# Kernel tuning notes

Hardware: AMD Instinct MI355X
Metric: run time of the kernel (lower is better)

The kernel has to match this reference:

```python
import jax, jax.numpy as jnp
import numpy as np

N = 50000      # nodes
E = 500000     # edges
D_IN = 64      # node_in_dim
K = 4          # edge_in_dim
H = 64         # node_hidden_dim
C = 40         # num_class
L = 2          # num_layers


def setup_inputs() -> dict:
    key = jax.random.key(0)
    ks = jax.random.split(key, 10)
    node_features = jax.random.normal(ks[0], (N, D_IN), jnp.float32)
    edge_features = jax.random.normal(ks[1], (L, E, K), jnp.float32)
    src = jax.random.randint(ks[2], (E,), 0, N)
    dst = jax.random.randint(ks[3], (E,), 0, N)
    W0 = jax.random.normal(ks[4], (K * D_IN, H), jnp.float32) * 0.05
    b0 = jnp.zeros((H,), jnp.float32)
    W1 = jax.random.normal(ks[5], (K * H, H), jnp.float32) * 0.05
    b1 = jnp.zeros((H,), jnp.float32)
    Wfc = jax.random.normal(ks[6], (H, C), jnp.float32) * 0.05
    bfc = jnp.zeros((C,), jnp.float32)
    return dict(node_features=node_features, edge_features=edge_features,
                src=src, dst=dst, W0=W0, b0=b0, W1=W1, b1=b1, Wfc=Wfc, bfc=bfc)


def reference(node_features, edge_features, src, dst, W0, b0, W1, b1, Wfc, bfc):
    h = node_features  # [N, d]
    ones = jnp.ones((E,), jnp.float32)
    cnt = jnp.maximum(jax.ops.segment_sum(ones, dst, num_segments=N), 1.0)  # in-degree
    for i, (W, b) in enumerate([(W0, b0), (W1, b1)]):
        e = edge_features[i]          # [E, K]
        hs = h[src]                   # [E, d] edge gather of src node features
        d = hs.shape[1]
        # message: relu(Linear(flatten(e[:,:,None] * h[:,None,:])))
        # flatten order is (K, d), so reshape W -> [K, d, H] and contract directly
        Wr = W.reshape(K, d, H)
        m = jax.nn.relu(jnp.einsum('ek,ed,kdh->eh', e, hs, Wr) + b)  # [E, H]
        s = jax.ops.segment_sum(m, dst, num_segments=N)              # scatter-sum
        h = jax.nn.relu(s / cnt[:, None])                            # mailbox mean + relu
    return h @ Wfc + bfc  # [N, C]
```

## Files before the change

### kernel.cpp

```cpp
#include <hip/hip_runtime.h>
#include <hip/hip_fp16.h>

#define N_NODES 50000
#define N_EDGES 500000
#define DIM 64
#define KDIM 4
#define HID 64
#define NCLS 40
#define NBLK ((N_NODES + 255) / 256)

__device__ inline unsigned pack2(float a, float b) {
    __half2 h = __floats2half2_rn(a, b);
    return *(unsigned*)&h;
}
__device__ inline float2 unpack2(unsigned u) {
    __half2 h = *(__half2*)&u;
    return __half22float2(h);
}

__global__ void hist_k(const int* __restrict__ dst, int* __restrict__ cnt) {
    int e = blockIdx.x * 256 + threadIdx.x;
    if (e < N_EDGES) atomicAdd(&cnt[dst[e]], 1);
}

__global__ __launch_bounds__(256) void blk_scan_k(const int* __restrict__ cnt,
                                                  int* __restrict__ esc,
                                                  int* __restrict__ bsum) {
    __shared__ int ls[256];
    int t = threadIdx.x;
    int n = blockIdx.x * 256 + t;
    int v = (n < N_NODES) ? cnt[n] : 0;
    ls[t] = v;
    __syncthreads();
#pragma unroll
    for (int off = 1; off < 256; off <<= 1) {
        int u = (t >= off) ? ls[t - off] : 0;
        __syncthreads();
        ls[t] += u;
        __syncthreads();
    }
    if (n < N_NODES) esc[n] = ls[t] - v;
    if (t == 255) bsum[blockIdx.x] = ls[255];
}

__global__ __launch_bounds__(256) void bsum_scan_k(const int* __restrict__ bsum,
                                                   int* __restrict__ boff,
                                                   int* __restrict__ start) {
    __shared__ int ls[256];
    int t = threadIdx.x;
    int v = (t < NBLK) ? bsum[t] : 0;
    ls[t] = v;
    __syncthreads();
#pragma unroll
    for (int off = 1; off < 256; off <<= 1) {
        int u = (t >= off) ? ls[t - off] : 0;
        __syncthreads();
        ls[t] += u;
        __syncthreads();
    }
    if (t < NBLK) boff[t] = ls[t] - v;
    if (t == 0) start[N_NODES] = N_EDGES;
}

__global__ void finalize_k(const int* __restrict__ esc, const int* __restrict__ boff,
                           int* __restrict__ start, int* __restrict__ cursor) {
    int n = blockIdx.x * 256 + threadIdx.x;
    if (n < N_NODES) {
        int s = esc[n] + boff[blockIdx.x];
        start[n] = s;
        cursor[n] = s;
    }
}

__global__ void scatter_k(const int* __restrict__ src, const int* __restrict__ dst,
                          const float* __restrict__ ef, int* __restrict__ cursor,
                          uint4* __restrict__ rec0, uint4* __restrict__ rec1) {
    int e = blockIdx.x * 256 + threadIdx.x;
    if (e < N_EDGES) {
        int d = dst[e];
        int pos = atomicAdd(&cursor[d], 1);
        int sn = src[e];
        float4 f0 = ((const float4*)ef)[e];
        float4 f1 = ((const float4*)ef)[N_EDGES + e];
        uint4 r0 = make_uint4((unsigned)sn, pack2(f0.x, f0.y), pack2(f0.z, f0.w), 0u);
        uint4 r1 = make_uint4((unsigned)sn, pack2(f1.x, f1.y), pack2(f1.z, f1.w), 0u);
        rec0[pos] = r0;
        rec1[pos] = r1;
    }
}

__global__ __launch_bounds__(256) void transform_k(const float* __restrict__ hin,
                                                   const float* __restrict__ W,
                                                   unsigned* __restrict__ y) {
    __shared__ float sW[KDIM * 64 * 64];
    __shared__ float sh[32 * 65];
    int t = threadIdx.x;

    const float4* W4 = (const float4*)W;
    float4* sW4 = (float4*)sW;
#pragma unroll
    for (int i = 0; i < 16; ++i) sW4[t + 256 * i] = W4[t + 256 * i];

    int n0 = blockIdx.x * 32;
#pragma unroll
    for (int i = 0; i < 2; ++i) {
        int idx = t + 256 * i;
        int nl = idx >> 4;
        int dg = idx & 15;
        int n = n0 + nl;
        float4 v = make_float4(0.f, 0.f, 0.f, 0.f);
        if (n < N_NODES) v = ((const float4*)hin)[(size_t)n * 16 + dg];
        sh[nl * 65 + dg * 4 + 0] = v.x;
        sh[nl * 65 + dg * 4 + 1] = v.y;
        sh[nl * 65 + dg * 4 + 2] = v.z;
        sh[nl * 65 + dg * 4 + 3] = v.w;
    }
    __syncthreads();

    int nl = t & 15;
    int cg = t >> 4;
    int k = cg >> 2;
    int hc0 = (cg & 3) * 16;

    float acc0[16], acc1[16];
#pragma unroll
    for (int j = 0; j < 16; ++j) { acc0[j] = 0.f; acc1[j] = 0.f; }

    for (int d = 0; d < 64; ++d) {
        float a0 = sh[nl * 65 + d];
        float a1 = sh[(nl + 16) * 65 + d];
        const float* wr = &sW[k * 4096 + d * 64 + hc0];
#pragma unroll
        for (int j = 0; j < 16; ++j) {
            float w = wr[j];
            acc0[j] = fmaf(a0, w, acc0[j]);
            acc1[j] = fmaf(a1, w, acc1[j]);
        }
    }

    int n_a = n0 + nl, n_b = n0 + nl + 16;
    int cbase = k * 64 + hc0;
    if (n_a < N_NODES) {
        uint4* o = (uint4*)(y + ((size_t)n_a * 256 + cbase) / 2);
        o[0] = make_uint4(pack2(acc0[0], acc0[1]), pack2(acc0[2], acc0[3]),
                          pack2(acc0[4], acc0[5]), pack2(acc0[6], acc0[7]));
        o[1] = make_uint4(pack2(acc0[8], acc0[9]), pack2(acc0[10], acc0[11]),
                          pack2(acc0[12], acc0[13]), pack2(acc0[14], acc0[15]));
    }
    if (n_b < N_NODES) {
        uint4* o = (uint4*)(y + ((size_t)n_b * 256 + cbase) / 2);
        o[0] = make_uint4(pack2(acc1[0], acc1[1]), pack2(acc1[2], acc1[3]),
                          pack2(acc1[4], acc1[5]), pack2(acc1[6], acc1[7]));
        o[1] = make_uint4(pack2(acc1[8], acc1[9]), pack2(acc1[10], acc1[11]),
                          pack2(acc1[12], acc1[13]), pack2(acc1[14], acc1[15]));
    }
}

__device__ inline void edge_step(const uint4 r, const unsigned* __restrict__ y,
                                 int lane, const float4 bias, float4& acc) {
    int sn = (int)r.x;
    float2 e01 = unpack2(r.y);
    float2 e23 = unpack2(r.z);
    const uint2* yb = (const uint2*)(y + (size_t)sn * 128);
    uint2 q0 = yb[lane];
    uint2 q1 = yb[16 + lane];
    uint2 q2 = yb[32 + lane];
    uint2 q3 = yb[48 + lane];

    float2 a0 = unpack2(q0.x), a1 = unpack2(q0.y);
    float2 b0 = unpack2(q1.x), b1 = unpack2(q1.y);
    float2 c0 = unpack2(q2.x), c1 = unpack2(q2.y);
    float2 d0 = unpack2(q3.x), d1 = unpack2(q3.y);

    float4 z = bias;
    z.x = fmaf(e01.x, a0.x, z.x); z.y = fmaf(e01.x, a0.y, z.y);
    z.z = fmaf(e01.x, a1.x, z.z); z.w = fmaf(e01.x, a1.y, z.w);
    z.x = fmaf(e01.y, b0.x, z.x); z.y = fmaf(e01.y, b0.y, z.y);
    z.z = fmaf(e01.y, b1.x, z.z); z.w = fmaf(e01.y, b1.y, z.w);
    z.x = fmaf(e23.x, c0.x, z.x); z.y = fmaf(e23.x, c0.y, z.y);
    z.z = fmaf(e23.x, c1.x, z.z); z.w = fmaf(e23.x, c1.y, z.w);
    z.x = fmaf(e23.y, d0.x, z.x); z.y = fmaf(e23.y, d0.y, z.y);
    z.z = fmaf(e23.y, d1.x, z.z); z.w = fmaf(e23.y, d1.y, z.w);

    acc.x += fmaxf(z.x, 0.f);
    acc.y += fmaxf(z.y, 0.f);
    acc.z += fmaxf(z.z, 0.f);
    acc.w += fmaxf(z.w, 0.f);
}

__global__ __launch_bounds__(256) void agg_k(const uint4* __restrict__ rec,
                                             const int* __restrict__ start,
                                             const int* __restrict__ cnt,
                                             const unsigned* __restrict__ y,
                                             const float* __restrict__ b,
                                             float* __restrict__ hout) {
    int t = blockIdx.x * 256 + threadIdx.x;
    int g = t >> 4;
    int lane = t & 15;
    if (g >= N_NODES) return;

    int s0 = start[g];
    int deg = cnt[g];
    int s1 = s0 + deg;

    float4 bias = ((const float4*)b)[lane];
    float4 acc = make_float4(0.f, 0.f, 0.f, 0.f);

    int i = s0;
    for (; i + 2 <= s1; i += 2) {
        uint4 r0 = rec[i];
        uint4 r1 = rec[i + 1];
        edge_step(r0, y, lane, bias, acc);
        edge_step(r1, y, lane, bias, acc);
    }
    if (i < s1) {
        uint4 r0 = rec[i];
        edge_step(r0, y, lane, bias, acc);
    }

    float inv = 1.0f / (float)(deg > 1 ? deg : 1);
    float4 r;
    r.x = fmaxf(acc.x * inv, 0.f);
    r.y = fmaxf(acc.y * inv, 0.f);
    r.z = fmaxf(acc.z * inv, 0.f);
    r.w = fmaxf(acc.w * inv, 0.f);
    ((float4*)hout)[(size_t)g * 16 + lane] = r;
}

__global__ void fc_k(const float* __restrict__ h, const float* __restrict__ Wfc,
                     const float* __restrict__ bfc, float* __restrict__ out) {
    int t = blockIdx.x * 256 + threadIdx.x;
    if (t >= N_NODES * NCLS) return;
    int n = t / NCLS;
    int c = t - n * NCLS;
    const float* hr = h + (size_t)n * 64;
    float acc = bfc[c];
#pragma unroll
    for (int j = 0; j < 64; ++j) acc = fmaf(hr[j], Wfc[j * NCLS + c], acc);
    out[t] = acc;
}

extern "C" void kernel_launch(void* const* d_in, const int* in_sizes, int n_in,
                              void* d_out, int out_size, void* d_ws, size_t ws_size,
                              hipStream_t stream) {
    const float* nf  = (const float*)d_in[0];
    const float* ef  = (const float*)d_in[1];
    const int*   src = (const int*)d_in[2];
    const int*   dst = (const int*)d_in[3];
    const float* W0  = (const float*)d_in[4];
    const float* b0  = (const float*)d_in[5];
    const float* W1  = (const float*)d_in[6];
    const float* b1  = (const float*)d_in[7];
    const float* Wfc = (const float*)d_in[8];
    const float* bfc = (const float*)d_in[9];
    float* out = (float*)d_out;

    char* ws = (char*)d_ws;
    size_t off = 0;
    auto alloc = [&](size_t bytes) -> void* {
        void* p = ws + off;
        off = (off + bytes + 255) & ~(size_t)255;
        return p;
    };
    int*      cnt    = (int*)     alloc((size_t)N_NODES * 4);
    int*      esc    = (int*)     alloc((size_t)N_NODES * 4);
    int*      bsum   = (int*)     alloc((size_t)NBLK * 4);
    int*      boff   = (int*)     alloc((size_t)NBLK * 4);
    int*      start  = (int*)     alloc((size_t)(N_NODES + 1) * 4);
    int*      cursor = (int*)     alloc((size_t)N_NODES * 4);
    uint4*    rec0   = (uint4*)   alloc((size_t)N_EDGES * 16);
    uint4*    rec1   = (uint4*)   alloc((size_t)N_EDGES * 16);
    unsigned* y      = (unsigned*)alloc((size_t)N_NODES * 256 * 2);
    float*    hbuf   = (float*)   alloc((size_t)N_NODES * 64 * 4);

    hipMemsetAsync(cnt, 0, (size_t)N_NODES * 4, stream);

    hist_k<<<(N_EDGES + 255) / 256, 256, 0, stream>>>(dst, cnt);
    blk_scan_k<<<NBLK, 256, 0, stream>>>(cnt, esc, bsum);
    bsum_scan_k<<<1, 256, 0, stream>>>(bsum, boff, start);
    finalize_k<<<NBLK, 256, 0, stream>>>(esc, boff, start, cursor);
    scatter_k<<<(N_EDGES + 255) / 256, 256, 0, stream>>>(src, dst, ef, cursor, rec0, rec1);

    int tgrid = (N_NODES + 31) / 32;
    int agrid = (N_NODES * 16 + 255) / 256;

    transform_k<<<tgrid, 256, 0, stream>>>(nf, W0, y);
    agg_k<<<agrid, 256, 0, stream>>>(rec0, start, cnt, y, b0, hbuf);

    transform_k<<<tgrid, 256, 0, stream>>>(hbuf, W1, y);
    agg_k<<<agrid, 256, 0, stream>>>(rec1, start, cnt, y, b1, hbuf);

    fc_k<<<(N_NODES * NCLS + 255) / 256, 256, 0, stream>>>(hbuf, Wfc, bfc, out);
}
```

Baseline: 322.3 us.

## Merge scan kernels via decoupled lookback, interleave edge records, fuse final FC

Replaces the three-kernel prefix scan with a single kernel in which each block publishes its total and spins on flags from all earlier blocks, removing two launches. The two per-layer edge record arrays are interleaved into one buffer, so each agg pass reads every other 16-byte record. The final FC is fused into the second aggregation kernel through shared memory, avoiding a separate launch and the hbuf round trip. Risks include the spin-wait relying on all earlier blocks being resident and halved record-stream efficiency in agg.

```diff
diff --git a/kernel.cpp b/kernel.cpp
--- a/kernel.cpp
+++ b/kernel.cpp
@@ -23,12 +23,16 @@
     if (e < N_EDGES) atomicAdd(&cnt[dst[e]], 1);
 }
 
-__global__ __launch_bounds__(256) void blk_scan_k(const int* __restrict__ cnt,
-                                                  int* __restrict__ esc,
-                                                  int* __restrict__ bsum) {
+__global__ __launch_bounds__(256) void scan_k(const int* __restrict__ cnt,
+                                              int* __restrict__ start,
+                                              int* __restrict__ cursor,
+                                              volatile int* __restrict__ bflag,
+                                              volatile int* __restrict__ bval) {
     __shared__ int ls[256];
-    int t = threadIdx.x;
-    int n = blockIdx.x * 256 + t;
+    __shared__ int sbase;
+    __shared__ int ok_all;
+    int b = blockIdx.x, t = threadIdx.x;
+    int n = b * 256 + t;
     int v = (n < N_NODES) ? cnt[n] : 0;
     ls[t] = v;
     __syncthreads();
@@ -39,42 +43,49 @@
         ls[t] += u;
         __syncthreads();
     }
-    if (n < N_NODES) esc[n] = ls[t] - v;
-    if (t == 255) bsum[blockIdx.x] = ls[255];
-}
-
-__global__ __launch_bounds__(256) void bsum_scan_k(const int* __restrict__ bsum,
-                                                   int* __restrict__ boff,
-                                                   int* __restrict__ start) {
-    __shared__ int ls[256];
-    int t = threadIdx.x;
-    int v = (t < NBLK) ? bsum[t] : 0;
-    ls[t] = v;
+    int incl = ls[t];
+    int total = ls[255];
     __syncthreads();
-#pragma unroll
-    for (int off = 1; off < 256; off <<= 1) {
-        int u = (t >= off) ? ls[t - off] : 0;
-        __syncthreads();
-        ls[t] += u;
-        __syncthreads();
-    }
-    if (t < NBLK) boff[t] = ls[t] - v;
-    if (t == 0) start[N_NODES] = N_EDGES;
-}
-
-__global__ void finalize_k(const int* __restrict__ esc, const int* __restrict__ boff,
-                           int* __restrict__ start, int* __restrict__ cursor) {
-    int n = blockIdx.x * 256 + threadIdx.x;
-    if (n < N_NODES) {
-        int s = esc[n] + boff[blockIdx.x];
-        start[n] = s;
-        cursor[n] = s;
-    }
+
+    if (t == 0) {
+        bval[b] = total;
+        __threadfence();
+        bflag[b] = 1;
+    }
+
+    if (b > 0) {
+        for (;;) {
+            int f = (t < b) ? bflag[t] : 1;
+            if (t == 0) ok_all = 1;
+            __syncthreads();
+            if (!f) ok_all = 0;
+            __syncthreads();
+            if (ok_all) break;
+        }
+        __threadfence();
+        int pv = (t < b) ? bval[t] : 0;
+        ls[t] = pv;
+        __syncthreads();
+#pragma unroll
+        for (int off = 128; off > 0; off >>= 1) {
+            if (t < off) ls[t] += ls[t + off];
+            __syncthreads();
+        }
+        if (t == 0) sbase = ls[0];
+        __syncthreads();
+    } else {
+        if (t == 0) sbase = 0;
+        __syncthreads();
+    }
+
+    int excl = sbase + incl - v;
+    if (n < N_NODES) { start[n] = excl; cursor[n] = excl; }
+    if (n == 0) start[N_NODES] = N_EDGES;
 }
 
 __global__ void scatter_k(const int* __restrict__ src, const int* __restrict__ dst,
                           const float* __restrict__ ef, int* __restrict__ cursor,
-                          uint4* __restrict__ rec0, uint4* __restrict__ rec1) {
+                          uint4* __restrict__ rec) {
     int e = blockIdx.x * 256 + threadIdx.x;
     if (e < N_EDGES) {
         int d = dst[e];
@@ -82,10 +93,8 @@
         int sn = src[e];
         float4 f0 = ((const float4*)ef)[e];
         float4 f1 = ((const float4*)ef)[N_EDGES + e];
-        uint4 r0 = make_uint4((unsigned)sn, pack2(f0.x, f0.y), pack2(f0.z, f0.w), 0u);
-        uint4 r1 = make_uint4((unsigned)sn, pack2(f1.x, f1.y), pack2(f1.z, f1.w), 0u);
-        rec0[pos] = r0;
-        rec1[pos] = r1;
+        rec[2 * pos]     = make_uint4((unsigned)sn, pack2(f0.x, f0.y), pack2(f0.z, f0.w), 0u);
+        rec[2 * pos + 1] = make_uint4((unsigned)sn, pack2(f1.x, f1.y), pack2(f1.z, f1.w), 0u);
     }
 }
 
@@ -188,7 +197,41 @@
     acc.w += fmaxf(z.w, 0.f);
 }
 
-__global__ __launch_bounds__(256) void agg_k(const uint4* __restrict__ rec,
+__device__ inline float4 agg_core(const uint4* __restrict__ rec2,
+                                  const int* __restrict__ start,
+                                  const int* __restrict__ cnt,
+                                  const unsigned* __restrict__ y,
+                                  const float* __restrict__ b,
+                                  int g, int lane) {
+    int s0 = start[g];
+    int deg = cnt[g];
+    int s1 = s0 + deg;
+
+    float4 bias = ((const float4*)b)[lane];
+    float4 acc = make_float4(0.f, 0.f, 0.f, 0.f);
+
+    int i = s0;
+    for (; i + 2 <= s1; i += 2) {
+        uint4 r0 = rec2[2 * i];
+        uint4 r1 = rec2[2 * (i + 1)];
+        edge_step(r0, y, lane, bias, acc);
+        edge_step(r1, y, lane, bias, acc);
+    }
+    if (i < s1) {
+        uint4 r0 = rec2[2 * i];
+        edge_step(r0, y, lane, bias, acc);
+    }
+
+    float inv = 1.0f / (float)(deg > 1 ? deg : 1);
+    float4 r;
+    r.x = fmaxf(acc.x * inv, 0.f);
+    r.y = fmaxf(acc.y * inv, 0.f);
+    r.z = fmaxf(acc.z * inv, 0.f);
+    r.w = fmaxf(acc.w * inv, 0.f);
+    return r;
+}
+
+__global__ __launch_bounds__(256) void agg_k(const uint4* __restrict__ rec2,
                                              const int* __restrict__ start,
                                              const int* __restrict__ cnt,
                                              const unsigned* __restrict__ y,
@@ -197,47 +240,46 @@
     int t = blockIdx.x * 256 + threadIdx.x;
     int g = t >> 4;
     int lane = t & 15;
-    if (g >= N_NODES) return;
-
-    int s0 = start[g];
-    int deg = cnt[g];
-    int s1 = s0 + deg;
-
-    float4 bias = ((const float4*)b)[lane];
-    float4 acc = make_float4(0.f, 0.f, 0.f, 0.f);
-
-    int i = s0;
-    for (; i + 2 <= s1; i += 2) {
-        uint4 r0 = rec[i];
-        uint4 r1 = rec[i + 1];
-        edge_step(r0, y, lane, bias, acc);
-        edge_step(r1, y, lane, bias, acc);
-    }
-    if (i < s1) {
-        uint4 r0 = rec[i];
-        edge_step(r0, y, lane, bias, acc);
-    }
-
-    float inv = 1.0f / (float)(deg > 1 ? deg : 1);
-    float4 r;
-    r.x = fmaxf(acc.x * inv, 0.f);
-    r.y = fmaxf(acc.y * inv, 0.f);
-    r.z = fmaxf(acc.z * inv, 0.f);
-    r.w = fmaxf(acc.w * inv, 0.f);
+    float4 r = agg_core(rec2, start, cnt, y, b, g, lane);
     ((float4*)hout)[(size_t)g * 16 + lane] = r;
 }
 
-__global__ void fc_k(const float* __restrict__ h, const float* __restrict__ Wfc,
-                     const float* __restrict__ bfc, float* __restrict__ out) {
-    int t = blockIdx.x * 256 + threadIdx.x;
-    if (t >= N_NODES * NCLS) return;
-    int n = t / NCLS;
-    int c = t - n * NCLS;
-    const float* hr = h + (size_t)n * 64;
-    float acc = bfc[c];
-#pragma unroll
-    for (int j = 0; j < 64; ++j) acc = fmaf(hr[j], Wfc[j * NCLS + c], acc);
-    out[t] = acc;
+__global__ __launch_bounds__(256) void agg_fc_k(const uint4* __restrict__ rec2,
+                                                const int* __restrict__ start,
+                                                const int* __restrict__ cnt,
+                                                const unsigned* __restrict__ y,
+                                                const float* __restrict__ b,
+                                                const float* __restrict__ Wfc,
+                                                const float* __restrict__ bfc,
+                                                float* __restrict__ out) {
+    __shared__ float sh_h[16 * 65];
+    __shared__ float sWfc[64 * NCLS];
+    __shared__ float sbfc[NCLS];
+    int t = threadIdx.x;
+
+    for (int i = t; i < 64 * NCLS; i += 256) sWfc[i] = Wfc[i];
+    if (t < NCLS) sbfc[t] = bfc[t];
+
+    int nl = t >> 4;
+    int lane = t & 15;
+    int g = blockIdx.x * 16 + nl;
+
+    float4 r = agg_core(rec2, start, cnt, y, b, g, lane);
+    sh_h[nl * 65 + lane * 4 + 0] = r.x;
+    sh_h[nl * 65 + lane * 4 + 1] = r.y;
+    sh_h[nl * 65 + lane * 4 + 2] = r.z;
+    sh_h[nl * 65 + lane * 4 + 3] = r.w;
+    __syncthreads();
+
+    for (int item = t; item < 16 * NCLS; item += 256) {
+        int rn = item / NCLS;
+        int c = item - rn * NCLS;
+        float acc = sbfc[c];
+        const float* hr = &sh_h[rn * 65];
+#pragma unroll
+        for (int j = 0; j < 64; ++j) acc = fmaf(hr[j], sWfc[j * NCLS + c], acc);
+        out[(size_t)(blockIdx.x * 16 + rn) * NCLS + c] = acc;
+    }
 }
 
 extern "C" void kernel_launch(void* const* d_in, const int* in_sizes, int n_in,
@@ -262,33 +304,28 @@
         off = (off + bytes + 255) & ~(size_t)255;
         return p;
     };
-    int*      cnt    = (int*)     alloc((size_t)N_NODES * 4);
-    int*      esc    = (int*)     alloc((size_t)N_NODES * 4);
-    int*      bsum   = (int*)     alloc((size_t)NBLK * 4);
-    int*      boff   = (int*)     alloc((size_t)NBLK * 4);
+    int*      zbuf   = (int*)     alloc((size_t)(50176 + 512) * 4);
+    int*      cnt    = zbuf;
+    int*      bflag  = zbuf + 50176;
+    int*      bval   = zbuf + 50176 + 256;
     int*      start  = (int*)     alloc((size_t)(N_NODES + 1) * 4);
     int*      cursor = (int*)     alloc((size_t)N_NODES * 4);
-    uint4*    rec0   = (uint4*)   alloc((size_t)N_EDGES * 16);
-    uint4*    rec1   = (uint4*)   alloc((size_t)N_EDGES * 16);
+    uint4*    rec    = (uint4*)   alloc((size_t)N_EDGES * 32);
     unsigned* y      = (unsigned*)alloc((size_t)N_NODES * 256 * 2);
     float*    hbuf   = (float*)   alloc((size_t)N_NODES * 64 * 4);
 
-    hipMemsetAsync(cnt, 0, (size_t)N_NODES * 4, stream);
+    hipMemsetAsync(zbuf, 0, (size_t)(50176 + 512) * 4, stream);
 
     hist_k<<<(N_EDGES + 255) / 256, 256, 0, stream>>>(dst, cnt);
-    blk_scan_k<<<NBLK, 256, 0, stream>>>(cnt, esc, bsum);
-    bsum_scan_k<<<1, 256, 0, stream>>>(bsum, boff, start);
-    finalize_k<<<NBLK, 256, 0, stream>>>(esc, boff, start, cursor);
-    scatter_k<<<(N_EDGES + 255) / 256, 256, 0, stream>>>(src, dst, ef, cursor, rec0, rec1);
+    scan_k<<<NBLK, 256, 0, stream>>>(cnt, start, cursor, bflag, bval);
+    scatter_k<<<(N_EDGES + 255) / 256, 256, 0, stream>>>(src, dst, ef, cursor, rec);
 
     int tgrid = (N_NODES + 31) / 32;
-    int agrid = (N_NODES * 16 + 255) / 256;
+    int agrid = N_NODES / 16;
 
     transform_k<<<tgrid, 256, 0, stream>>>(nf, W0, y);
-    agg_k<<<agrid, 256, 0, stream>>>(rec0, start, cnt, y, b0, hbuf);
+    agg_k<<<agrid, 256, 0, stream>>>(rec, start, cnt, y, b0, hbuf);
 
     transform_k<<<tgrid, 256, 0, stream>>>(hbuf, W1, y);
-    agg_k<<<agrid, 256, 0, stream>>>(rec1, start, cnt, y, b1, hbuf);
-
-    fc_k<<<(N_NODES * NCLS + 255) / 256, 256, 0, stream>>>(hbuf, Wfc, bfc, out);
-}
+    agg_fc_k<<<agrid, 256, 0, stream>>>(rec + 1, start, cnt, y, b1, Wfc, bfc, out);
+}
```

Result: faster. 308.6 us (-4.2%).
